# Optimization experiments

Hardware: AMD Instinct MI355X
Metric: run time of the kernel (lower is better)

## Reference

```python
import jax, jax.numpy as jnp
import numpy as np

# Placement-region / binning constants (init args of DensityPotential)
XL, YL, XH, YH = 0.0, 0.0, 512.0, 512.0
BIN = 1.0                      # bin_size_x == bin_size_y
NBX = int(np.ceil((XH - XL) / BIN))   # 512
NBY = int(np.ceil((YH - YL) / BIN))   # 512
K = 5                          # num_impacted_bins = ceil((max_size + 4*bin)/bin), max_size<=1
TARGET_DENSITY = 0.9
N = 1_000_000                  # movable + filler nodes (num_terminals = 0)


def setup_inputs() -> dict:
    key = jax.random.key(0)
    k1, k2, k3, k4 = jax.random.split(key, 4)
    sx = 0.5 + 0.5 * jax.random.uniform(k1, (N,), dtype=jnp.float32)
    sy = 0.5 + 0.5 * jax.random.uniform(k2, (N,), dtype=jnp.float32)
    # node lower-left corners, kept inside the region
    x = jax.random.uniform(k3, (N,), dtype=jnp.float32, minval=XL, maxval=XH - 1.0)
    y = jax.random.uniform(k4, (N,), dtype=jnp.float32, minval=YL, maxval=YH - 1.0)
    pos = jnp.concatenate([x, y])  # DREAMPlace layout: [x ; y]
    # NTUPlace3 bell-shape coefficients (per node)
    ax = 4.0 / ((sx + 2 * BIN) * (sx + 4 * BIN))
    bx = 2.0 / (BIN * (sx + 4 * BIN))
    cx = sx
    ay = 4.0 / ((sy + 2 * BIN) * (sy + 4 * BIN))
    by = 2.0 / (BIN * (sy + 4 * BIN))
    cy = sy
    bin_center_x = (XL + (jnp.arange(NBX, dtype=jnp.float32) + 0.5) * BIN)
    bin_center_y = (YL + (jnp.arange(NBY, dtype=jnp.float32) + 0.5) * BIN)
    initial_density_map = jnp.zeros((NBX, NBY), dtype=jnp.float32)  # num_terminals == 0
    return dict(pos=pos, node_size_x=sx, node_size_y=sy,
                ax=ax, bx=bx, cx=cx, ay=ay, by=by, cy=cy,
                bin_center_x=bin_center_x, bin_center_y=bin_center_y,
                initial_density_map=initial_density_map)


def _axis_potential(coord, size, a, b, c, bin_center, nbins, lo):
    """Per-node 1D NTUPlace3 bell-shaped potential over its K impacted bins.
    Returns (idx [N,K] int32, pot [N,K] float)."""
    center = coord + 0.5 * size                               # cell center
    # first impacted bin: window covers centers within size/2 + 2*bin of center
    start = jnp.floor((coord - 2.0 * BIN - lo) / BIN).astype(jnp.int32)
    start = jnp.clip(start, 0, nbins - K)                     # keep all K indices valid
    idx = start[:, None] + jnp.arange(K, dtype=jnp.int32)[None, :]  # [N,K]
    dist = jnp.abs(center[:, None] - bin_center[idx])         # [N,K]
    p1 = (0.5 * size + BIN)[:, None]
    p2 = (0.5 * size + 2.0 * BIN)[:, None]
    pot = jnp.where(dist < p1,
                    c[:, None] * (1.0 - a[:, None] * dist * dist),
                    jnp.where(dist < p2,
                              (c * b)[:, None] * (dist - p2) ** 2,
                              jnp.zeros_like(dist)))
    return idx, pot


def reference(pos, node_size_x, node_size_y, ax, bx, cx, ay, by, cy,
              bin_center_x, bin_center_y, initial_density_map):
    n = node_size_x.shape[0]
    x, y = pos[:n], pos[n:]
    ix, px = _axis_potential(x, node_size_x, ax, bx, cx, bin_center_x, NBX, XL)
    iy, py = _axis_potential(y, node_size_y, ay, by, cy, bin_center_y, NBY, YL)
    # separable 2D splat: contribution to bin (i,j) is px_i * py_j
    flat_idx = (ix[:, :, None] * NBY + iy[:, None, :]).reshape(-1)   # [N*K*K]
    vals = (px[:, :, None] * py[:, None, :]).reshape(-1)             # [N*K*K]
    density_map = initial_density_map.reshape(-1).at[flat_idx].add(vals)
    density_map = density_map.reshape(NBX, NBY)
    target_area = TARGET_DENSITY * BIN * BIN
    delta = density_map - target_area
    cost = jnp.sum(delta * delta)   # NTUPlace3 quadratic density potential
    return cost
```

## Files before the change

kernel.cpp:

```cpp
#include <hip/hip_runtime.h>

#define NBX 512
#define NBY 512
#define KNB 5
#define NMAP (NBX * NBY)
#define TARGET_AREA 0.9f

#define TSH 5
#define TS 32
#define NTX 16
#define NTY 16
#define NT (NTX * NTY)
#define HALO 2
#define RDIM (TS + 2 * HALO)
#define RWORDS (RDIM * RDIM)
#define BPT 2
#define NSLAB (BPT * 4)
#define KCH 256
#define USTR 264
#define UVHALFS (48 * USTR)

typedef _Float16 f16x8 __attribute__((ext_vector_type(8)));
typedef float f32x4 __attribute__((ext_vector_type(4)));

__device__ __forceinline__ unsigned short f2h(float f) {
    return __builtin_bit_cast(unsigned short, (_Float16)f);
}

__device__ __forceinline__ void compute_node(
    float x, float y, float sx, float sy,
    float a_x, float b_x, float c_x,
    float a_y, float b_y, float c_y,
    int& rsx, int& rsy, float* px, float* py)
{
    float ctrx = x + 0.5f * sx;
    float ctry = y + 0.5f * sy;
    rsx = min(max((int)floorf(x - 2.0f), 0), NBX - KNB);
    rsy = min(max((int)floorf(y - 2.0f), 0), NBY - KNB);
    float p1x = 0.5f * sx + 1.0f, p2x = 0.5f * sx + 2.0f;
    float p1y = 0.5f * sy + 1.0f, p2y = 0.5f * sy + 2.0f;
#pragma unroll
    for (int k = 0; k < KNB; ++k) {
        float d = fabsf(ctrx - ((float)(rsx + k) + 0.5f));
        float dm = d - p2x;
        float v1 = c_x * (1.0f - a_x * d * d);
        float v2 = (c_x * b_x) * dm * dm;
        px[k] = (d < p1x) ? v1 : ((d < p2x) ? v2 : 0.0f);
    }
#pragma unroll
    for (int k = 0; k < KNB; ++k) {
        float d = fabsf(ctry - ((float)(rsy + k) + 0.5f));
        float dm = d - p2y;
        float v1 = c_y * (1.0f - a_y * d * d);
        float v2 = (c_y * b_y) * dm * dm;
        py[k] = (d < p1y) ? v1 : ((d < p2y) ? v2 : 0.0f);
    }
}

__device__ __forceinline__ int tile_of(int rsx, int rsy) {
    int tx = (rsx + HALO) >> TSH;
    int ty = (rsy + HALO) >> TSH;
    return tx * NTY + ty;
}

__global__ __launch_bounds__(1024) void count_kernel(
    const float* __restrict__ pos, int* __restrict__ counts, int n, int B1)
{
    __shared__ int hist[NT];
    for (int t = threadIdx.x; t < NT; t += 1024) hist[t] = 0;
    __syncthreads();
    int i = blockIdx.x * 1024 + threadIdx.x;
    if (i < n) {
        float x = pos[i], y = pos[n + i];
        int rsx = min(max((int)floorf(x - 2.0f), 0), NBX - KNB);
        int rsy = min(max((int)floorf(y - 2.0f), 0), NBY - KNB);
        atomicAdd(&hist[tile_of(rsx, rsy)], 1);
    }
    __syncthreads();
    for (int t = threadIdx.x; t < NT; t += 1024)
        counts[t * B1 + blockIdx.x] = hist[t];
}

__global__ __launch_bounds__(256) void scan1_kernel(
    const int* __restrict__ counts, int* __restrict__ base,
    int* __restrict__ partials, int L)
{
    __shared__ int ls[256];
    int tid = threadIdx.x;
    int i0 = blockIdx.x * 1024 + tid * 4;
    int v[4], s = 0;
#pragma unroll
    for (int k = 0; k < 4; ++k) { v[k] = (i0 + k < L) ? counts[i0 + k] : 0; s += v[k]; }
    ls[tid] = s;
    __syncthreads();
    for (int off = 1; off < 256; off <<= 1) {
        int t = (tid >= off) ? ls[tid - off] : 0;
        __syncthreads();
        ls[tid] += t;
        __syncthreads();
    }
    int excl = ls[tid] - s;
    int run = excl;
#pragma unroll
    for (int k = 0; k < 4; ++k) { if (i0 + k < L) base[i0 + k] = run; run += v[k]; }
    if (tid == 255) partials[blockIdx.x] = ls[255];
}

__global__ __launch_bounds__(256) void scan2_kernel(int* __restrict__ partials, int G)
{
    __shared__ int ls[256];
    int tid = threadIdx.x;
    int i0 = tid * 4;
    int v[4], s = 0;
#pragma unroll
    for (int k = 0; k < 4; ++k) { v[k] = (i0 + k < G) ? partials[i0 + k] : 0; s += v[k]; }
    ls[tid] = s;
    __syncthreads();
    for (int off = 1; off < 256; off <<= 1) {
        int t = (tid >= off) ? ls[tid - off] : 0;
        __syncthreads();
        ls[tid] += t;
        __syncthreads();
    }
    int excl = ls[tid] - s;
    int run = excl;
#pragma unroll
    for (int k = 0; k < 4; ++k) { if (i0 + k < G) partials[i0 + k] = run; run += v[k]; }
}

__global__ __launch_bounds__(1024) void scatter_kernel(
    const float* __restrict__ pos,
    const float* __restrict__ nsx, const float* __restrict__ nsy,
    const float* __restrict__ axp, const float* __restrict__ bxp, const float* __restrict__ cxp,
    const float* __restrict__ ayp, const float* __restrict__ byp, const float* __restrict__ cyp,
    const int* __restrict__ base, const int* __restrict__ partials,
    uint4* __restrict__ records, int n, int B1)
{
    __shared__ int lcur[NT];
    int tid = threadIdx.x;
    for (int t = tid; t < NT; t += 1024) lcur[t] = 0;
    __syncthreads();
    int i = blockIdx.x * 1024 + tid;
    if (i >= n) return;

    float x = pos[i], y = pos[n + i];
    int rsx, rsy;
    float px[KNB], py[KNB];
    compute_node(x, y, nsx[i], nsy[i], axp[i], bxp[i], cxp[i],
                 ayp[i], byp[i], cyp[i], rsx, rsy, px, py);
    int tile = tile_of(rsx, rsy);
    int rank = atomicAdd(&lcur[tile], 1);
    int p = tile * B1 + blockIdx.x;
    int slot = base[p] + partials[p >> 10] + rank;

    unsigned h[10];
#pragma unroll
    for (int k = 0; k < KNB; ++k) h[k] = f2h(px[k]);
#pragma unroll
    for (int k = 0; k < KNB; ++k) h[KNB + k] = f2h(py[k]);

    uint4* rec = records + (size_t)slot * 2;
    rec[0] = make_uint4((unsigned)rsx | ((unsigned)rsy << 16),
                        h[0] | (h[1] << 16), h[2] | (h[3] << 16), h[4] | (h[5] << 16));
    rec[1] = make_uint4(h[6] | (h[7] << 16), h[8] | (h[9] << 16), 0u, 0u);
}

__global__ __launch_bounds__(256) void accum_mfma_kernel(
    const uint4* __restrict__ records,
    const int* __restrict__ base, const int* __restrict__ partials,
    float* __restrict__ scratch, int n, int B1)
{
    __shared__ __align__(16) unsigned short UV[2 * UVHALFS];
    int blk = blockIdx.x;
    int tile = blk / BPT, sub = blk % BPT;
    int tx = tile / NTY, ty = tile % NTY;
    int tid = threadIdx.x;
    int lane = tid & 63, w = tid >> 6;

    int p0 = tile * B1;
    int off0 = base[p0] + partials[p0 >> 10];
    int off1 = (tile == NT - 1) ? n : (base[p0 + B1] + partials[(p0 + B1) >> 10]);
    int cnt = off1 - off0;
    int c0 = off0 + (int)(((long long)cnt * sub) / BPT);
    int c1 = off0 + (int)(((long long)cnt * (sub + 1)) / BPT);
    int nch = (c1 - c0 + KCH - 1) / KCH;

    f32x4 acc[9];
#pragma unroll
    for (int t = 0; t < 9; ++t) acc[t] = (f32x4){0.f, 0.f, 0.f, 0.f};

    uint4 r0, r1;
    bool valid = (c0 + tid) < c1;
    if (valid) {
        const uint4* rp = records + (size_t)(c0 + tid) * 2;
        r0 = rp[0]; r1 = rp[1];
    }

    for (int ch = 0; ch < nch; ++ch) {
        uint4* z = (uint4*)UV;
#pragma unroll 2
        for (int q = tid; q < (2 * UVHALFS) / 8; q += 256)
            z[q] = make_uint4(0u, 0u, 0u, 0u);
        __syncthreads();

        if (valid) {
            int rs = (int)r0.x;
            int rsx = rs & 0xffff, rsy = rs >> 16;
            int lx = rsx + HALO - (tx << TSH);
            int ly = rsy + HALO - (ty << TSH);
            int k = tid;
            unsigned short hx[5], hy[5];
            hx[0] = (unsigned short)r0.y; hx[1] = (unsigned short)(r0.y >> 16);
            hx[2] = (unsigned short)r0.z; hx[3] = (unsigned short)(r0.z >> 16);
            hx[4] = (unsigned short)r0.w; hy[0] = (unsigned short)(r0.w >> 16);
            hy[1] = (unsigned short)r1.x; hy[2] = (unsigned short)(r1.x >> 16);
            hy[3] = (unsigned short)r1.y; hy[4] = (unsigned short)(r1.y >> 16);
#pragma unroll
            for (int i2 = 0; i2 < KNB; ++i2)
                UV[(lx + i2) * USTR + k] = hx[i2];
#pragma unroll
            for (int i2 = 0; i2 < KNB; ++i2)
                UV[UVHALFS + (ly + i2) * USTR + k] = hy[i2];
        }

        int jn = c0 + (ch + 1) * KCH + tid;
        bool valid_n = jn < c1;
        uint4 r0n, r1n;
        if (valid_n) {
            const uint4* rp = records + (size_t)jn * 2;
            r0n = rp[0]; r1n = rp[1];
        }
        __syncthreads();

        int mrow = lane & 15, quad = lane >> 4;
#pragma unroll
        for (int kk = 0; kk < 2; ++kk) {
            int kbase = w * 64 + kk * 32 + quad * 8;
#pragma unroll
            for (int ti = 0; ti < 3; ++ti) {
                const f16x8* pa = (const f16x8*)&UV[(ti * 16 + mrow) * USTR + kbase];
                f16x8 a = *pa;
#pragma unroll
                for (int tj = 0; tj < 3; ++tj) {
                    const f16x8* pb = (const f16x8*)&UV[UVHALFS + (tj * 16 + mrow) * USTR + kbase];
                    acc[ti * 3 + tj] = __builtin_amdgcn_mfma_f32_16x16x32_f16(
                        a, *pb, acc[ti * 3 + tj], 0, 0, 0);
                }
            }
        }
        __syncthreads();

        r0 = r0n; r1 = r1n; valid = valid_n;
    }

    float* slab = scratch + ((size_t)(tile * BPT + sub) * 4 + w) * RWORDS;
    int col = lane & 15, quad = lane >> 4;
#pragma unroll
    for (int ti = 0; ti < 3; ++ti) {
#pragma unroll
        for (int tj = 0; tj < 3; ++tj) {
            int ly = tj * 16 + col;
#pragma unroll
            for (int r = 0; r < 4; ++r) {
                int lx = ti * 16 + quad * 4 + r;
                if (lx < RDIM && ly < RDIM)
                    slab[lx * RDIM + ly] = acc[ti * 3 + tj][r];
            }
        }
    }
}

__global__ __launch_bounds__(256) void cost_kernel(
    const float* __restrict__ scratch, const float* __restrict__ initial_map,
    float* __restrict__ out)
{
    float acc = 0.0f;
    int stride = gridDim.x * blockDim.x;
    for (int b = blockIdx.x * blockDim.x + threadIdx.x; b < NMAP; b += stride) {
        int gx = b >> 9, gy = b & (NBY - 1);
        float d = initial_map[b] - TARGET_AREA;
        int txlo = max((gx - 2) >> 5, 0);
        int txhi = min((gx + 2) >> 5, NTX - 1);
        int tylo = max((gy - 2) >> 5, 0);
        int tyhi = min((gy + 2) >> 5, NTY - 1);
        for (int tx = txlo; tx <= txhi; ++tx) {
            int lx = gx - (tx << TSH) + HALO;
            for (int ty = tylo; ty <= tyhi; ++ty) {
                int ly = gy - (ty << TSH) + HALO;
                const float* s0 = scratch +
                    ((size_t)(tx * NTY + ty) * NSLAB) * RWORDS + lx * RDIM + ly;
#pragma unroll
                for (int s = 0; s < NSLAB; ++s) d += s0[(size_t)s * RWORDS];
            }
        }
        acc += d * d;
    }
#pragma unroll
    for (int off = 32; off > 0; off >>= 1)
        acc += __shfl_down(acc, off, 64);
    __shared__ float smem[4];
    int lane = threadIdx.x & 63;
    int wave = threadIdx.x >> 6;
    if (lane == 0) smem[wave] = acc;
    __syncthreads();
    if (threadIdx.x == 0)
        atomicAdd(out, smem[0] + smem[1] + smem[2] + smem[3]);
}

__global__ __launch_bounds__(256) void fallback_scatter_kernel(
    const float* __restrict__ pos,
    const float* __restrict__ nsx, const float* __restrict__ nsy,
    const float* __restrict__ axp, const float* __restrict__ bxp, const float* __restrict__ cxp,
    const float* __restrict__ ayp, const float* __restrict__ byp, const float* __restrict__ cyp,
    float* __restrict__ map, int n)
{
    int i = blockIdx.x * blockDim.x + threadIdx.x;
    if (i >= n) return;
    int rsx, rsy;
    float px[KNB], py[KNB];
    compute_node(pos[i], pos[n + i], nsx[i], nsy[i], axp[i], bxp[i], cxp[i],
                 ayp[i], byp[i], cyp[i], rsx, rsy, px, py);
#pragma unroll
    for (int kx = 0; kx < KNB; ++kx) {
        int rowbase = (rsx + kx) * NBY + rsy;
#pragma unroll
        for (int ky = 0; ky < KNB; ++ky)
            atomicAdd(&map[rowbase + ky], px[kx] * py[ky]);
    }
}

__global__ __launch_bounds__(256) void fallback_cost_kernel(
    const float* __restrict__ map, const float* __restrict__ initial_map,
    float* __restrict__ out)
{
    float acc = 0.0f;
    int stride = gridDim.x * blockDim.x;
    for (int b = blockIdx.x * blockDim.x + threadIdx.x; b < NMAP; b += stride) {
        float d = map[b] + initial_map[b] - TARGET_AREA;
        acc += d * d;
    }
#pragma unroll
    for (int off = 32; off > 0; off >>= 1)
        acc += __shfl_down(acc, off, 64);
    __shared__ float smem[4];
    int lane = threadIdx.x & 63;
    int wave = threadIdx.x >> 6;
    if (lane == 0) smem[wave] = acc;
    __syncthreads();
    if (threadIdx.x == 0)
        atomicAdd(out, smem[0] + smem[1] + smem[2] + smem[3]);
}

extern "C" void kernel_launch(void* const* d_in, const int* in_sizes, int n_in,
                              void* d_out, int out_size, void* d_ws, size_t ws_size,
                              hipStream_t stream) {
    const float* pos = (const float*)d_in[0];
    const float* nsx = (const float*)d_in[1];
    const float* nsy = (const float*)d_in[2];
    const float* axp = (const float*)d_in[3];
    const float* bxp = (const float*)d_in[4];
    const float* cxp = (const float*)d_in[5];
    const float* ayp = (const float*)d_in[6];
    const float* byp = (const float*)d_in[7];
    const float* cyp = (const float*)d_in[8];
    const float* initial_map = (const float*)d_in[11];

    int n = in_sizes[1];
    int B1 = (n + 1023) >> 10;
    int L  = NT * B1;
    int G  = (L + 1023) >> 10;

    size_t off_base   = (size_t)L * 4;
    size_t off_part   = off_base + (size_t)L * 4;
    size_t off_rec    = (off_part + (size_t)G * 4 + 255) & ~(size_t)255;
    size_t rec_bytes  = (size_t)n * 32;
    size_t off_scr    = (off_rec + rec_bytes + 255) & ~(size_t)255;
    size_t scratch_sz = (size_t)NT * NSLAB * RWORDS * 4;
    size_t need = off_scr + scratch_sz;

    int*   counts   = (int*)d_ws;
    int*   basep    = (int*)((char*)d_ws + off_base);
    int*   partials = (int*)((char*)d_ws + off_part);
    uint4* records  = (uint4*)((char*)d_ws + off_rec);
    float* scratch  = (float*)((char*)d_ws + off_scr);

    hipMemsetAsync(d_out, 0, sizeof(float), stream);

    if (ws_size >= need && G <= 1024) {
        count_kernel<<<B1, 1024, 0, stream>>>(pos, counts, n, B1);
        scan1_kernel<<<G, 256, 0, stream>>>(counts, basep, partials, L);
        scan2_kernel<<<1, 256, 0, stream>>>(partials, G);
        scatter_kernel<<<B1, 1024, 0, stream>>>(
            pos, nsx, nsy, axp, bxp, cxp, ayp, byp, cyp,
            basep, partials, records, n, B1);
        accum_mfma_kernel<<<NT * BPT, 256, 0, stream>>>(
            records, basep, partials, scratch, n, B1);
        cost_kernel<<<256, 256, 0, stream>>>(scratch, initial_map, (float*)d_out);
    } else {
        float* map = (float*)d_ws;
        hipMemsetAsync(d_ws, 0, (size_t)NMAP * 4, stream);
        fallback_scatter_kernel<<<(n + 255) / 256, 256, 0, stream>>>(
            pos, nsx, nsy, axp, bxp, cxp, ayp, byp, cyp, map, n);
        fallback_cost_kernel<<<256, 256, 0, stream>>>(map, initial_map, (float*)d_out);
    }
}
```

Baseline: 155.0 us.

## Replace count/scan/scatter pipeline with fused fixed-capacity tile bucketing and overflow map

Removes the count pass and the two scan kernels. A single fused scatter kernel builds a per-block histogram, reserves slots with a global atomic on each tile cursor, and writes records into fixed-capacity per-tile buckets. Nodes that overflow a bucket go to a global float map through atomics. The MFMA accumulation kernel zeroes LDS once and then clears only the rows the previous chunk wrote. It also reduces the four wave slabs in LDS so each block writes one slab, which cuts the scratch reads in the cost kernel. The trade-off is a larger fixed record buffer, a memset of the overflow map, and nondeterministic slot order.

```diff
diff --git a/kernel.cpp b/kernel.cpp
--- a/kernel.cpp
+++ b/kernel.cpp
@@ -15,10 +15,10 @@
 #define RDIM (TS + 2 * HALO)
 #define RWORDS (RDIM * RDIM)
 #define BPT 2
-#define NSLAB (BPT * 4)
 #define KCH 256
 #define USTR 264
 #define UVHALFS (48 * USTR)
+#define CAP 6144
 
 typedef _Float16 f16x8 __attribute__((ext_vector_type(8)));
 typedef float f32x4 __attribute__((ext_vector_type(4)));
@@ -63,112 +63,67 @@
     return tx * NTY + ty;
 }
 
-__global__ __launch_bounds__(1024) void count_kernel(
-    const float* __restrict__ pos, int* __restrict__ counts, int n, int B1)
-{
-    __shared__ int hist[NT];
-    for (int t = threadIdx.x; t < NT; t += 1024) hist[t] = 0;
-    __syncthreads();
-    int i = blockIdx.x * 1024 + threadIdx.x;
-    if (i < n) {
-        float x = pos[i], y = pos[n + i];
-        int rsx = min(max((int)floorf(x - 2.0f), 0), NBX - KNB);
-        int rsy = min(max((int)floorf(y - 2.0f), 0), NBY - KNB);
-        atomicAdd(&hist[tile_of(rsx, rsy)], 1);
-    }
-    __syncthreads();
-    for (int t = threadIdx.x; t < NT; t += 1024)
-        counts[t * B1 + blockIdx.x] = hist[t];
-}
-
-__global__ __launch_bounds__(256) void scan1_kernel(
-    const int* __restrict__ counts, int* __restrict__ base,
-    int* __restrict__ partials, int L)
-{
-    __shared__ int ls[256];
-    int tid = threadIdx.x;
-    int i0 = blockIdx.x * 1024 + tid * 4;
-    int v[4], s = 0;
-#pragma unroll
-    for (int k = 0; k < 4; ++k) { v[k] = (i0 + k < L) ? counts[i0 + k] : 0; s += v[k]; }
-    ls[tid] = s;
-    __syncthreads();
-    for (int off = 1; off < 256; off <<= 1) {
-        int t = (tid >= off) ? ls[tid - off] : 0;
-        __syncthreads();
-        ls[tid] += t;
-        __syncthreads();
-    }
-    int excl = ls[tid] - s;
-    int run = excl;
-#pragma unroll
-    for (int k = 0; k < 4; ++k) { if (i0 + k < L) base[i0 + k] = run; run += v[k]; }
-    if (tid == 255) partials[blockIdx.x] = ls[255];
-}
-
-__global__ __launch_bounds__(256) void scan2_kernel(int* __restrict__ partials, int G)
-{
-    __shared__ int ls[256];
-    int tid = threadIdx.x;
-    int i0 = tid * 4;
-    int v[4], s = 0;
-#pragma unroll
-    for (int k = 0; k < 4; ++k) { v[k] = (i0 + k < G) ? partials[i0 + k] : 0; s += v[k]; }
-    ls[tid] = s;
-    __syncthreads();
-    for (int off = 1; off < 256; off <<= 1) {
-        int t = (tid >= off) ? ls[tid - off] : 0;
-        __syncthreads();
-        ls[tid] += t;
-        __syncthreads();
-    }
-    int excl = ls[tid] - s;
-    int run = excl;
-#pragma unroll
-    for (int k = 0; k < 4; ++k) { if (i0 + k < G) partials[i0 + k] = run; run += v[k]; }
-}
-
-__global__ __launch_bounds__(1024) void scatter_kernel(
+__global__ __launch_bounds__(1024) void scatter_fused_kernel(
     const float* __restrict__ pos,
     const float* __restrict__ nsx, const float* __restrict__ nsy,
     const float* __restrict__ axp, const float* __restrict__ bxp, const float* __restrict__ cxp,
     const float* __restrict__ ayp, const float* __restrict__ byp, const float* __restrict__ cyp,
-    const int* __restrict__ base, const int* __restrict__ partials,
-    uint4* __restrict__ records, int n, int B1)
-{
-    __shared__ int lcur[NT];
+    int* __restrict__ cursors, float* __restrict__ ovmap,
+    uint4* __restrict__ records, int n)
+{
+    __shared__ int hist[NT];
+    __shared__ int hbase[NT];
     int tid = threadIdx.x;
-    for (int t = tid; t < NT; t += 1024) lcur[t] = 0;
-    __syncthreads();
+    if (tid < NT) hist[tid] = 0;
+    __syncthreads();
+
     int i = blockIdx.x * 1024 + tid;
-    if (i >= n) return;
-
-    float x = pos[i], y = pos[n + i];
-    int rsx, rsy;
+    bool act = i < n;
+    int rsx = 0, rsy = 0, tile = 0;
     float px[KNB], py[KNB];
-    compute_node(x, y, nsx[i], nsy[i], axp[i], bxp[i], cxp[i],
-                 ayp[i], byp[i], cyp[i], rsx, rsy, px, py);
-    int tile = tile_of(rsx, rsy);
-    int rank = atomicAdd(&lcur[tile], 1);
-    int p = tile * B1 + blockIdx.x;
-    int slot = base[p] + partials[p >> 10] + rank;
-
-    unsigned h[10];
-#pragma unroll
-    for (int k = 0; k < KNB; ++k) h[k] = f2h(px[k]);
-#pragma unroll
-    for (int k = 0; k < KNB; ++k) h[KNB + k] = f2h(py[k]);
-
-    uint4* rec = records + (size_t)slot * 2;
-    rec[0] = make_uint4((unsigned)rsx | ((unsigned)rsy << 16),
-                        h[0] | (h[1] << 16), h[2] | (h[3] << 16), h[4] | (h[5] << 16));
-    rec[1] = make_uint4(h[6] | (h[7] << 16), h[8] | (h[9] << 16), 0u, 0u);
+    if (act) {
+        compute_node(pos[i], pos[n + i], nsx[i], nsy[i], axp[i], bxp[i], cxp[i],
+                     ayp[i], byp[i], cyp[i], rsx, rsy, px, py);
+        tile = tile_of(rsx, rsy);
+        atomicAdd(&hist[tile], 1);
+    }
+    __syncthreads();
+
+    if (tid < NT) {
+        int c = hist[tid];
+        hbase[tid] = c ? atomicAdd(&cursors[tid], c) : 0;
+        hist[tid] = 0;
+    }
+    __syncthreads();
+
+    if (act) {
+        int rank = atomicAdd(&hist[tile], 1);
+        int slot = hbase[tile] + rank;
+        if (slot < CAP) {
+            unsigned h[10];
+#pragma unroll
+            for (int k = 0; k < KNB; ++k) h[k] = f2h(px[k]);
+#pragma unroll
+            for (int k = 0; k < KNB; ++k) h[KNB + k] = f2h(py[k]);
+            uint4* rec = records + ((size_t)tile * CAP + slot) * 2;
+            rec[0] = make_uint4((unsigned)rsx | ((unsigned)rsy << 16),
+                                h[0] | (h[1] << 16), h[2] | (h[3] << 16), h[4] | (h[5] << 16));
+            rec[1] = make_uint4(h[6] | (h[7] << 16), h[8] | (h[9] << 16), 0u, 0u);
+        } else {
+#pragma unroll
+            for (int kx = 0; kx < KNB; ++kx) {
+                int rowbase = (rsx + kx) * NBY + rsy;
+#pragma unroll
+                for (int ky = 0; ky < KNB; ++ky)
+                    atomicAdd(&ovmap[rowbase + ky], px[kx] * py[ky]);
+            }
+        }
+    }
 }
 
 __global__ __launch_bounds__(256) void accum_mfma_kernel(
-    const uint4* __restrict__ records,
-    const int* __restrict__ base, const int* __restrict__ partials,
-    float* __restrict__ scratch, int n, int B1)
+    const uint4* __restrict__ records, const int* __restrict__ cursors,
+    float* __restrict__ scratch)
 {
     __shared__ __align__(16) unsigned short UV[2 * UVHALFS];
     int blk = blockIdx.x;
@@ -177,38 +132,43 @@
     int tid = threadIdx.x;
     int lane = tid & 63, w = tid >> 6;
 
-    int p0 = tile * B1;
-    int off0 = base[p0] + partials[p0 >> 10];
-    int off1 = (tile == NT - 1) ? n : (base[p0 + B1] + partials[(p0 + B1) >> 10]);
-    int cnt = off1 - off0;
-    int c0 = off0 + (int)(((long long)cnt * sub) / BPT);
-    int c1 = off0 + (int)(((long long)cnt * (sub + 1)) / BPT);
+    int cnt = min(cursors[tile], CAP);
+    int c0 = (int)(((long long)cnt * sub) / BPT);
+    int c1 = (int)(((long long)cnt * (sub + 1)) / BPT);
     int nch = (c1 - c0 + KCH - 1) / KCH;
+    const uint4* rbase = records + (size_t)tile * CAP * 2;
 
     f32x4 acc[9];
 #pragma unroll
     for (int t = 0; t < 9; ++t) acc[t] = (f32x4){0.f, 0.f, 0.f, 0.f};
+
+    {
+        uint4* z = (uint4*)UV;
+        for (int q = tid; q < (2 * UVHALFS) / 8; q += 256)
+            z[q] = make_uint4(0u, 0u, 0u, 0u);
+    }
 
     uint4 r0, r1;
     bool valid = (c0 + tid) < c1;
-    if (valid) {
-        const uint4* rp = records + (size_t)(c0 + tid) * 2;
-        r0 = rp[0]; r1 = rp[1];
-    }
+    if (valid) { const uint4* rp = rbase + (size_t)(c0 + tid) * 2; r0 = rp[0]; r1 = rp[1]; }
+    __syncthreads();
+
+    int plx = 0, ply = 0;
+    bool have_prev = false;
 
     for (int ch = 0; ch < nch; ++ch) {
-        uint4* z = (uint4*)UV;
-#pragma unroll 2
-        for (int q = tid; q < (2 * UVHALFS) / 8; q += 256)
-            z[q] = make_uint4(0u, 0u, 0u, 0u);
-        __syncthreads();
-
+        if (have_prev) {
+#pragma unroll
+            for (int i2 = 0; i2 < KNB; ++i2) UV[(plx + i2) * USTR + tid] = 0;
+#pragma unroll
+            for (int i2 = 0; i2 < KNB; ++i2) UV[UVHALFS + (ply + i2) * USTR + tid] = 0;
+        }
+        have_prev = false;
         if (valid) {
             int rs = (int)r0.x;
             int rsx = rs & 0xffff, rsy = rs >> 16;
             int lx = rsx + HALO - (tx << TSH);
             int ly = rsy + HALO - (ty << TSH);
-            int k = tid;
             unsigned short hx[5], hy[5];
             hx[0] = (unsigned short)r0.y; hx[1] = (unsigned short)(r0.y >> 16);
             hx[2] = (unsigned short)r0.z; hx[3] = (unsigned short)(r0.z >> 16);
@@ -216,20 +176,16 @@
             hy[1] = (unsigned short)r1.x; hy[2] = (unsigned short)(r1.x >> 16);
             hy[3] = (unsigned short)r1.y; hy[4] = (unsigned short)(r1.y >> 16);
 #pragma unroll
-            for (int i2 = 0; i2 < KNB; ++i2)
-                UV[(lx + i2) * USTR + k] = hx[i2];
-#pragma unroll
-            for (int i2 = 0; i2 < KNB; ++i2)
-                UV[UVHALFS + (ly + i2) * USTR + k] = hy[i2];
+            for (int i2 = 0; i2 < KNB; ++i2) UV[(lx + i2) * USTR + tid] = hx[i2];
+#pragma unroll
+            for (int i2 = 0; i2 < KNB; ++i2) UV[UVHALFS + (ly + i2) * USTR + tid] = hy[i2];
+            plx = lx; ply = ly; have_prev = true;
         }
 
         int jn = c0 + (ch + 1) * KCH + tid;
         bool valid_n = jn < c1;
         uint4 r0n, r1n;
-        if (valid_n) {
-            const uint4* rp = records + (size_t)jn * 2;
-            r0n = rp[0]; r1n = rp[1];
-        }
+        if (valid_n) { const uint4* rp = rbase + (size_t)jn * 2; r0n = rp[0]; r1n = rp[1]; }
         __syncthreads();
 
         int mrow = lane & 15, quad = lane >> 4;
@@ -253,32 +209,53 @@
         r0 = r0n; r1 = r1n; valid = valid_n;
     }
 
-    float* slab = scratch + ((size_t)(tile * BPT + sub) * 4 + w) * RWORDS;
+    float* F = (float*)UV;
     int col = lane & 15, quad = lane >> 4;
-#pragma unroll
-    for (int ti = 0; ti < 3; ++ti) {
-#pragma unroll
-        for (int tj = 0; tj < 3; ++tj) {
-            int ly = tj * 16 + col;
-#pragma unroll
-            for (int r = 0; r < 4; ++r) {
-                int lx = ti * 16 + quad * 4 + r;
-                if (lx < RDIM && ly < RDIM)
-                    slab[lx * RDIM + ly] = acc[ti * 3 + tj][r];
-            }
-        }
-    }
+    if ((w & 1) == 0) {
+        float* R = F + (w >> 1) * RWORDS;
+#pragma unroll
+        for (int ti = 0; ti < 3; ++ti)
+#pragma unroll
+            for (int tj = 0; tj < 3; ++tj) {
+                int ly = tj * 16 + col;
+#pragma unroll
+                for (int r = 0; r < 4; ++r) {
+                    int lx = ti * 16 + quad * 4 + r;
+                    if (lx < RDIM && ly < RDIM) R[lx * RDIM + ly] = acc[ti * 3 + tj][r];
+                }
+            }
+    }
+    __syncthreads();
+    if ((w & 1) == 1) {
+        float* R = F + (w >> 1) * RWORDS;
+#pragma unroll
+        for (int ti = 0; ti < 3; ++ti)
+#pragma unroll
+            for (int tj = 0; tj < 3; ++tj) {
+                int ly = tj * 16 + col;
+#pragma unroll
+                for (int r = 0; r < 4; ++r) {
+                    int lx = ti * 16 + quad * 4 + r;
+                    if (lx < RDIM && ly < RDIM) R[lx * RDIM + ly] += acc[ti * 3 + tj][r];
+                }
+            }
+    }
+    __syncthreads();
+    for (int q = tid; q < RWORDS; q += 256) F[q] += F[RWORDS + q];
+    __syncthreads();
+    float* slab = scratch + (size_t)blk * RWORDS;
+    for (int q = tid; q < RWORDS; q += 256) slab[q] = F[q];
 }
 
 __global__ __launch_bounds__(256) void cost_kernel(
-    const float* __restrict__ scratch, const float* __restrict__ initial_map,
-    float* __restrict__ out)
+    const float* __restrict__ scratch, const float* __restrict__ ovmap,
+    const float* __restrict__ initial_map, float* __restrict__ out)
 {
     float acc = 0.0f;
     int stride = gridDim.x * blockDim.x;
     for (int b = blockIdx.x * blockDim.x + threadIdx.x; b < NMAP; b += stride) {
         int gx = b >> 9, gy = b & (NBY - 1);
-        float d = initial_map[b] - TARGET_AREA;
+        float d = initial_map[b] + ovmap[b] - TARGET_AREA;
         int txlo = max((gx - 2) >> 5, 0);
         int txhi = min((gx + 2) >> 5, NTX - 1);
         int tylo = max((gy - 2) >> 5, 0);
@@ -288,9 +265,9 @@
             for (int ty = tylo; ty <= tyhi; ++ty) {
                 int ly = gy - (ty << TSH) + HALO;
                 const float* s0 = scratch +
-                    ((size_t)(tx * NTY + ty) * NSLAB) * RWORDS + lx * RDIM + ly;
-#pragma unroll
-                for (int s = 0; s < NSLAB; ++s) d += s0[(size_t)s * RWORDS];
+                    ((size_t)(tx * NTY + ty) * BPT) * RWORDS + lx * RDIM + ly;
+#pragma unroll
+                for (int s = 0; s < BPT; ++s) d += s0[(size_t)s * RWORDS];
             }
         }
         acc += d * d;
@@ -367,35 +344,28 @@
 
     int n = in_sizes[1];
     int B1 = (n + 1023) >> 10;
-    int L  = NT * B1;
-    int G  = (L + 1023) >> 10;
-
-    size_t off_base   = (size_t)L * 4;
-    size_t off_part   = off_base + (size_t)L * 4;
-    size_t off_rec    = (off_part + (size_t)G * 4 + 255) & ~(size_t)255;
-    size_t rec_bytes  = (size_t)n * 32;
-    size_t off_scr    = (off_rec + rec_bytes + 255) & ~(size_t)255;
-    size_t scratch_sz = (size_t)NT * NSLAB * RWORDS * 4;
-    size_t need = off_scr + scratch_sz;
-
-    int*   counts   = (int*)d_ws;
-    int*   basep    = (int*)((char*)d_ws + off_base);
-    int*   partials = (int*)((char*)d_ws + off_part);
-    uint4* records  = (uint4*)((char*)d_ws + off_rec);
-    float* scratch  = (float*)((char*)d_ws + off_scr);
+
+    size_t off_ov   = (size_t)NT * 4;
+    size_t off_rec  = (off_ov + (size_t)NMAP * 4 + 255) & ~(size_t)255;
+    size_t rec_sz   = (size_t)NT * CAP * 32;
+    size_t off_scr  = (off_rec + rec_sz + 255) & ~(size_t)255;
+    size_t scr_sz   = (size_t)NT * BPT * RWORDS * 4;
+    size_t need     = off_scr + scr_sz;
+
+    int*   cursors = (int*)d_ws;
+    float* ovmap   = (float*)((char*)d_ws + off_ov);
+    uint4* records = (uint4*)((char*)d_ws + off_rec);
+    float* scratch = (float*)((char*)d_ws + off_scr);
 
     hipMemsetAsync(d_out, 0, sizeof(float), stream);
 
-    if (ws_size >= need && G <= 1024) {
-        count_kernel<<<B1, 1024, 0, stream>>>(pos, counts, n, B1);
-        scan1_kernel<<<G, 256, 0, stream>>>(counts, basep, partials, L);
-        scan2_kernel<<<1, 256, 0, stream>>>(partials, G);
-        scatter_kernel<<<B1, 1024, 0, stream>>>(
+    if (ws_size >= need) {
+        hipMemsetAsync(d_ws, 0, off_ov + (size_t)NMAP * 4, stream);
+        scatter_fused_kernel<<<B1, 1024, 0, stream>>>(
             pos, nsx, nsy, axp, bxp, cxp, ayp, byp, cyp,
-            basep, partials, records, n, B1);
-        accum_mfma_kernel<<<NT * BPT, 256, 0, stream>>>(
-            records, basep, partials, scratch, n, B1);
-        cost_kernel<<<256, 256, 0, stream>>>(scratch, initial_map, (float*)d_out);
+            cursors, ovmap, records, n);
+        accum_mfma_kernel<<<NT * BPT, 256, 0, stream>>>(records, cursors, scratch);
+        cost_kernel<<<256, 256, 0, stream>>>(scratch, ovmap, initial_map, (float*)d_out);
     } else {
         float* map = (float*)d_ws;
         hipMemsetAsync(d_ws, 0, (size_t)NMAP * 4, stream);
```

New measurement: 145.6 us. 1.07x faster.
